# Kernel tuning notes

Measured on AMD Instinct MI355X. Metric: run time of the kernel, lower is better.

Reference implementation:

```python
import jax, jax.numpy as jnp
import numpy as np
from jax import lax

B_, L_, EMB, VOCAB, NL, NH, CH = 4, 2048, 256, 256, 2, 8, 64
D_INNER = 2 * EMB          # expand=2
D_STATE = EMB              # d_state=emb_dim per source
D_CONV = 4
CONV_DIM = D_INNER + 2 * D_STATE
D_PROJ = 2 * D_INNER + 2 * D_STATE + NH
OUT_DIM = 256
EPS = 1e-5


def rms_norm(x, w):
    return x * lax.rsqrt(jnp.mean(x * x, axis=-1, keepdims=True) + EPS) * w


def segsum(a):
    # a: [..., T] -> [..., T, T] with entry (i,j) = sum a[j+1..i], -inf above diag
    T = a.shape[-1]
    cs = jnp.cumsum(a, axis=-1)
    seg = cs[..., :, None] - cs[..., None, :]
    mask = jnp.tril(jnp.ones((T, T), bool))
    return jnp.where(mask, seg, -jnp.inf)


def ssd(x, A, Bm, Cm, chunk):
    # x: [b,l,h,p], A: [b,l,h], Bm/Cm: [b,l,n] (ngroups=1, broadcast over heads)
    b, l, h, p = x.shape
    c = l // chunk
    x = x.reshape(b, c, chunk, h, p)
    A = A.reshape(b, c, chunk, h).transpose(0, 3, 1, 2)  # b h c l
    Bm = Bm.reshape(b, c, chunk, -1)
    Cm = Cm.reshape(b, c, chunk, -1)
    A_cs = jnp.cumsum(A, axis=-1)                        # b h c l
    L = jnp.exp(segsum(A))                               # b h c l l
    Y_diag = jnp.einsum("bcln,bcsn,bhcls,bcshp->bclhp", Cm, Bm, L, x)
    decay_states = jnp.exp(A_cs[..., -1:] - A_cs)        # b h c l
    states = jnp.einsum("bcln,bhcl,bclhp->bchpn", Bm, decay_states, x)
    states = jnp.concatenate([jnp.zeros_like(states[:, :1]), states], axis=1)  # b c+1 h p n
    decay_chunk = jnp.exp(segsum(jnp.pad(A_cs[:, :, :, -1], ((0, 0), (0, 0), (1, 0)))))  # b h c+1 c+1
    new_states = jnp.einsum("bhzc,bchpn->bzhpn", decay_chunk, states)
    states = new_states[:, :-1]                          # b c h p n
    Y_off = jnp.einsum("bcln,bchpn,bhcl->bclhp", Cm, states, jnp.exp(A_cs))
    return (Y_diag + Y_off).reshape(b, l, h, p)


def mamba2_block(u, in_proj_w, conv_w, conv_b, dt_bias, A_log, D, gnorm_w, outp_w):
    b, l, _ = u.shape
    zxbcdt = u @ in_proj_w                               # [b,l,D_PROJ]
    z = zxbcdt[..., :D_INNER]
    xBC = zxbcdt[..., D_INNER:D_INNER + CONV_DIM]
    dt = jax.nn.softplus(zxbcdt[..., -NH:] + dt_bias)    # [b,l,h]
    # causal depthwise conv1d, kernel 4
    xc = lax.conv_general_dilated(
        xBC.transpose(0, 2, 1), conv_w[:, None, :], (1,), [(D_CONV - 1, 0)],
        feature_group_count=CONV_DIM, dimension_numbers=("NCH", "OIH", "NCH"))
    xBC = jax.nn.silu(xc.transpose(0, 2, 1) + conv_b)
    xh = xBC[..., :D_INNER].reshape(b, l, NH, -1)        # [b,l,h,p]
    Bm = xBC[..., D_INNER:D_INNER + D_STATE]
    Cm = xBC[..., D_INNER + D_STATE:]
    A = -jnp.exp(A_log)                                  # [h]
    y = ssd(xh * dt[..., None], A * dt, Bm, Cm, CH)
    y = y + xh * D[:, None]
    y = y.reshape(b, l, D_INNER)
    y = rms_norm(y * jax.nn.silu(z), gnorm_w)
    return y @ outp_w


def _forward(idx, emb, in_proj_w, conv_w, conv_b, dt_bias, A_log, D,
             gnorm_w, outp_w, norm_w, normf_w, head_w):
    h = emb[idx]
    for i in range(NL):
        y = mamba2_block(rms_norm(h, norm_w[i]), in_proj_w[i], conv_w[i], conv_b[i],
                         dt_bias[i], A_log[i], D[i], gnorm_w[i], outp_w[i])
        h = y + h
    h = rms_norm(h, normf_w)
    return h @ head_w


def setup_inputs() -> dict:
    key = jax.random.key(0)
    ks = jax.random.split(key, 13)
    s = 0.02
    return {
        "x": jax.random.uniform(ks[0], (B_, L_, 1), jnp.float32),
        "emb": jax.random.normal(ks[1], (VOCAB, EMB)) * s,
        "in_proj_w": jax.random.normal(ks[2], (NL, EMB, D_PROJ)) * s,
        "conv_w": jax.random.normal(ks[3], (NL, CONV_DIM, D_CONV)) * 0.2,
        "conv_b": jax.random.normal(ks[4], (NL, CONV_DIM)) * s,
        "dt_bias": jax.random.normal(ks[5], (NL, NH)) * 0.1,
        "A_log": jnp.log(jax.random.uniform(ks[6], (NL, NH), minval=0.5, maxval=8.0)),
        "D": jax.random.normal(ks[7], (NL, NH)) * 0.5,
        "gnorm_w": 1.0 + jax.random.normal(ks[8], (NL, D_INNER)) * s,
        "outp_w": jax.random.normal(ks[9], (NL, D_INNER, EMB)) * s,
        "norm_w": 1.0 + jax.random.normal(ks[10], (NL, EMB)) * s,
        "normf_w": 1.0 + jax.random.normal(ks[11], (EMB,)) * s,
        "head_w": jax.random.normal(ks[12], (EMB, OUT_DIM)) * s,
    }


def reference(x, emb, in_proj_w, conv_w, conv_b, dt_bias, A_log, D,
              gnorm_w, outp_w, norm_w, normf_w, head_w):
    idx = jnp.clip(((VOCAB - 1) * x).astype(jnp.int32).squeeze(-1), 0, VOCAB - 1)
    return _forward(idx, emb, in_proj_w, conv_w, conv_b, dt_bias, A_log, D,
                    gnorm_w, outp_w, norm_w, normf_w, head_w)
```

## Files before the change

kernel.cpp:

```cpp
#include <hip/hip_runtime.h>
#include <cstddef>

#define NB 4
#define LSEQ 2048
#define BL (NB*LSEQ)
#define EMBD 256
#define DPROJ 1544
#define ZSTR 1600
#define DIN 512
#define DSTATE 256
#define CONVD 1024
#define NHD 8
#define PD 64
#define NC 32
#define NLAY 2
#define EPS 1e-5f

typedef __bf16 bf16x8 __attribute__((ext_vector_type(8)));
typedef float f32x4 __attribute__((ext_vector_type(4)));
typedef unsigned short u16;

__device__ float g_h [(size_t)BL*EMBD];
__device__ u16   g_ub[(size_t)BL*EMBD];
__device__ float g_zx[(size_t)BL*ZSTR];
__device__ u16   g_xbcb[(size_t)BL*CONVD];
__device__ float g_dt[(size_t)BL*NHD];
__device__ float g_acs[(size_t)NB*NHD*LSEQ];
__device__ float g_dAl[(size_t)NB*NHD*NC];
__device__ float g_y [(size_t)BL*DIN];
__device__ u16   g_yb[(size_t)BL*DIN];
__device__ u16   g_Sb[(size_t)NB*NC*NHD*PD*DSTATE];
__device__ u16   g_wt1[(size_t)ZSTR*EMBD];
__device__ u16   g_wt2[(size_t)EMBD*DIN];
__device__ u16   g_wt3[(size_t)EMBD*EMBD];

__device__ inline u16 f2b(float f){
  unsigned u = __float_as_uint(f);
  return (u16)((u + 0x7fffu + ((u>>16)&1u)) >> 16);
}
__device__ inline float b2f(u16 v){
  return __uint_as_float(((unsigned)v) << 16);
}

__global__ void k_embed(const float* __restrict__ x, const float* __restrict__ emb) {
  int i = blockIdx.x*256 + threadIdx.x;
  int row = i >> 8, col = i & 255;
  int idx = (int)(255.0f * x[row]);
  idx = idx < 0 ? 0 : (idx > 255 ? 255 : idx);
  g_h[i] = emb[idx*EMBD + col];
}

__global__ void k_rmsnorm(const float* __restrict__ in, const float* __restrict__ w,
                          u16* __restrict__ out) {
  int row = blockIdx.x, t = threadIdx.x;
  float v = in[(size_t)row*EMBD + t];
  float ss = v*v;
  #pragma unroll
  for (int o=32;o>0;o>>=1) ss += __shfl_down(ss,o,64);
  __shared__ float ls[4];
  if ((t&63)==0) ls[t>>6]=ss;
  __syncthreads();
  float tot = ls[0]+ls[1]+ls[2]+ls[3];
  float r = rsqrtf(tot*(1.0f/EMBD) + EPS);
  out[(size_t)row*EMBD + t] = f2b(v*r*w[t]);
}

__global__ void k_wt(const float* __restrict__ W, u16* __restrict__ WT, int K, int N) {
  __shared__ float t[64][65];
  int n0 = blockIdx.x*64, k0 = blockIdx.y*64;
  int tid = threadIdx.x;
  #pragma unroll
  for (int e=0;e<16;e++){
    int idx = tid + e*256;
    int kk = idx>>6, nn = idx&63;
    t[kk][nn] = (n0+nn < N) ? W[(size_t)(k0+kk)*N + n0+nn] : 0.f;
  }
  __syncthreads();
  #pragma unroll
  for (int e=0;e<16;e++){
    int idx = tid + e*256;
    int nn = idx>>6, kk = idx&63;
    WT[(size_t)(n0+nn)*K + k0+kk] = f2b(t[kk][nn]);
  }
}

template<int K, bool RES>
__global__ __launch_bounds__(256) void k_mfma_gemm(
    const u16* __restrict__ A, const u16* __restrict__ WT,
    const float* __restrict__ addC, float* __restrict__ C, int nstride)
{
  __shared__ u16 sA[128*64];
  __shared__ u16 sB[64*64];
  const int tid = threadIdx.x;
  const int lane = tid & 63;
  const int w = tid >> 6;
  const int bm = blockIdx.y * 128;
  const int bn = blockIdx.x * 64;
  const int r15 = lane & 15, kg = lane >> 4;
  f32x4 acc[2][4] = {};
  for (int k0 = 0; k0 < K; k0 += 64) {
    #pragma unroll
    for (int it = 0; it < 4; ++it) {
      int ch = it*256 + tid;
      int row = ch >> 3, c16 = ch & 7;
      uint4 v = *(const uint4*)(A + (size_t)(bm+row)*K + k0 + c16*8);
      *(uint4*)(sA + row*64 + ((c16 ^ (row&7))*8)) = v;
    }
    #pragma unroll
    for (int it = 0; it < 2; ++it) {
      int ch = it*256 + tid;
      int row = ch >> 3, c16 = ch & 7;
      uint4 v = *(const uint4*)(WT + (size_t)(bn+row)*K + k0 + c16*8);
      *(uint4*)(sB + row*64 + ((c16 ^ (row&7))*8)) = v;
    }
    __syncthreads();
    #pragma unroll
    for (int ks = 0; ks < 2; ++ks) {
      bf16x8 af[2], bfr[4];
      #pragma unroll
      for (int mr = 0; mr < 2; ++mr) {
        int row = w*32 + mr*16 + r15;
        int c16 = ks*4 + kg;
        af[mr] = *(const bf16x8*)(sA + row*64 + ((c16 ^ (row&7))*8));
      }
      #pragma unroll
      for (int nr = 0; nr < 4; ++nr) {
        int row = nr*16 + r15;
        int c16 = ks*4 + kg;
        bfr[nr] = *(const bf16x8*)(sB + row*64 + ((c16 ^ (row&7))*8));
      }
      #pragma unroll
      for (int mr = 0; mr < 2; ++mr)
        #pragma unroll
        for (int nr = 0; nr < 4; ++nr)
          acc[mr][nr] = __builtin_amdgcn_mfma_f32_16x16x32_bf16(af[mr], bfr[nr], acc[mr][nr], 0, 0, 0);
    }
    __syncthreads();
  }
  #pragma unroll
  for (int mr = 0; mr < 2; ++mr)
    #pragma unroll
    for (int j = 0; j < 4; ++j) {
      int grow = bm + w*32 + mr*16 + (lane>>4)*4 + j;
      #pragma unroll
      for (int nr = 0; nr < 4; ++nr) {
        int gcol = bn + nr*16 + (lane & 15);
        float v = acc[mr][nr][j];
        if (RES) v += addC[(size_t)grow*nstride + gcol];
        C[(size_t)grow*nstride + gcol] = v;
      }
    }
}

__global__ void k_dtscan(const float* __restrict__ dtb, const float* __restrict__ alog) {
  int gid = blockIdx.x;
  int cix = gid & (NC-1), bh = gid >> 5;
  int b = bh >> 3, h = bh & 7;
  int t = threadIdx.x;
  int row = b*LSEQ + cix*64 + t;
  float v = g_zx[(size_t)row*ZSTR + 1536 + h] + dtb[h];
  float sp = (v > 20.f) ? v : log1pf(__expf(v));
  g_dt[(size_t)row*NHD + h] = sp;
  float a = -__expf(alog[h]) * sp;
  #pragma unroll
  for (int o=1;o<64;o<<=1){
    float p = __shfl_up(a,o,64);
    if (t>=o) a += p;
  }
  g_acs[(size_t)bh*LSEQ + cix*64 + t] = a;
  if (t==63) g_dAl[(size_t)bh*NC + cix] = a;
}

__global__ __launch_bounds__(256) void k_conv(const float* __restrict__ cw,
                                              const float* __restrict__ cb) {
  int r0 = blockIdx.x * 4;
  int t0 = r0 & (LSEQ-1);
  int c  = threadIdx.x * 4;
  f32x4 v[7];
  #pragma unroll
  for (int i = 0; i < 7; ++i) {
    int tr = t0 - 3 + i;
    if (tr >= 0)
      v[i] = *(const f32x4*)(&g_zx[(size_t)(r0-3+i)*ZSTR + DIN + c]);
    else
      v[i] = (f32x4){0.f,0.f,0.f,0.f};
  }
  f32x4 w0 = *(const f32x4*)(&cw[(c+0)*4]);
  f32x4 w1 = *(const f32x4*)(&cw[(c+1)*4]);
  f32x4 w2 = *(const f32x4*)(&cw[(c+2)*4]);
  f32x4 w3 = *(const f32x4*)(&cw[(c+3)*4]);
  f32x4 bi = *(const f32x4*)(&cb[c]);
  #pragma unroll
  for (int j = 0; j < 4; ++j) {
    float o[4];
    #pragma unroll
    for (int ch = 0; ch < 4; ++ch) {
      const f32x4& wv = (ch==0)?w0:(ch==1)?w1:(ch==2)?w2:w3;
      float acc = bi[ch];
      #pragma unroll
      for (int k = 0; k < 4; ++k) acc += wv[k] * v[j+k][ch];
      o[ch] = acc / (1.f + __expf(-acc));
    }
    u16 o16[4];
    #pragma unroll
    for (int ch = 0; ch < 4; ++ch) o16[ch] = f2b(o[ch]);
    *(uint2*)(&g_xbcb[(size_t)(r0+j)*CONVD + c]) = *(const uint2*)o16;
  }
}

__global__ __launch_bounds__(512) void k_ssd1(const float* __restrict__ Dp) {
  int g = blockIdx.x;
  int h = g & 7, bc = g >> 3;
  int b = bc >> 5, cix = bc & 31;
  int row0 = b*LSEQ + cix*64;
  int bh = b*NHD + h;
  int tid = threadIdx.x;
  int lane = tid & 63, w = tid >> 6;
  int r15 = lane & 15, kq = lane >> 4;

  __shared__ u16 sBmt[256*64];
  __shared__ u16 sXt [64*64];
  __shared__ u16 sXdt[64*64];
  __shared__ u16 sM  [64*64];
  __shared__ float sAc[64];

  {
    int l = tid & 63;
    #pragma unroll
    for (int it = 0; it < 4; ++it) {
      int nc = (tid >> 6) + it*8;
      uint4 v4 = *(const uint4*)(&g_xbcb[(size_t)(row0+l)*CONVD + 512 + nc*8]);
      const u16* hp = (const u16*)&v4;
      #pragma unroll
      for (int i = 0; i < 8; ++i) {
        int n = nc*8 + i;
        sBmt[n*64 + (((l>>3) ^ (n&7))<<3) + (l&7)] = hp[i];
      }
    }
  }
  {
    int s = tid & 63, pc = tid >> 6;
    float ac  = g_acs[(size_t)bh*LSEQ + cix*64 + s];
    float dal = g_dAl[(size_t)bh*NC + cix];
    float dtv = g_dt[(size_t)(row0+s)*NHD + h];
    float dec = __expf(dal - ac);
    if (pc == 0) sAc[s] = ac;
    uint4 v4 = *(const uint4*)(&g_xbcb[(size_t)(row0+s)*CONVD + h*64 + pc*8]);
    const u16* hp = (const u16*)&v4;
    #pragma unroll
    for (int i = 0; i < 8; ++i) {
      int p = pc*8 + i;
      float xv = b2f(hp[i]) * dtv;
      int sw = (((s>>3) ^ (p&7))<<3) + (s&7);
      sXt [p*64 + sw] = f2b(xv);
      sXdt[p*64 + sw] = f2b(xv*dec);
    }
  }
  __syncthreads();

  {
    int S0  = (w >> 1)*16;
    int L0a = ((2*w) & 3)*16, L0b = L0a + 16;
    f32x4 acc0 = {}, acc1 = {};
    const u16* Ab = &g_xbcb[(size_t)(row0+S0 +r15)*CONVD + 512];
    const u16* B0 = &g_xbcb[(size_t)(row0+L0a+r15)*CONVD + 768];
    const u16* B1 = &g_xbcb[(size_t)(row0+L0b+r15)*CONVD + 768];
    #pragma unroll
    for (int ks = 0; ks < 8; ++ks) {
      int off = (ks*4 + kq)*8;
      bf16x8 af = *(const bf16x8*)(Ab + off);
      bf16x8 b0 = *(const bf16x8*)(B0 + off);
      bf16x8 b1 = *(const bf16x8*)(B1 + off);
      acc0 = __builtin_amdgcn_mfma_f32_16x16x32_bf16(af, b0, acc0, 0, 0, 0);
      acc1 = __builtin_amdgcn_mfma_f32_16x16x32_bf16(af, b1, acc1, 0, 0, 0);
    }
    int l0 = L0a + r15, l1 = L0b + r15;
    float acl0 = sAc[l0], acl1 = sAc[l1];
    #pragma unroll
    for (int j = 0; j < 4; ++j) {
      int s_ = S0 + kq*4 + j;
      float acs_ = sAc[s_];
      float m0 = (s_ <= l0) ? acc0[j]*__expf(acl0 - acs_) : 0.f;
      float m1 = (s_ <= l1) ? acc1[j]*__expf(acl1 - acs_) : 0.f;
      sM[l0*64 + (((s_>>3) ^ (l0&7))<<3) + (s_&7)] = f2b(m0);
      sM[l1*64 + (((s_>>3) ^ (l1&7))<<3) + (s_&7)] = f2b(m1);
    }
  }
  __syncthreads();

  {
    int lt = w >> 1;
    int pt0 = (2*w) & 3;
    int L0 = lt*16, P0 = pt0*16;
    f32x4 acc0 = {}, acc1 = {};
    #pragma unroll
    for (int ks = 0; ks < 2; ++ks) {
      int ch = ks*4 + kq;
      int sw = (ch ^ (r15&7))<<3;
      bf16x8 af = *(const bf16x8*)(&sM [(L0+r15)*64 + sw]);
      bf16x8 b0 = *(const bf16x8*)(&sXt[(P0+r15)*64 + sw]);
      bf16x8 b1 = *(const bf16x8*)(&sXt[(P0+16+r15)*64 + sw]);
      acc0 = __builtin_amdgcn_mfma_f32_16x16x32_bf16(af, b0, acc0, 0, 0, 0);
      acc1 = __builtin_amdgcn_mfma_f32_16x16x32_bf16(af, b1, acc1, 0, 0, 0);
    }
    float Dv = Dp[h];
    #pragma unroll
    for (int j = 0; j < 4; ++j) {
      int l = L0 + kq*4 + j;
      int p0 = P0 + r15, p1 = p0 + 16;
      float xh0 = b2f(g_xbcb[(size_t)(row0+l)*CONVD + h*64 + p0]);
      float xh1 = b2f(g_xbcb[(size_t)(row0+l)*CONVD + h*64 + p1]);
      g_y[(size_t)(row0+l)*DIN + h*64 + p0] = acc0[j] + Dv*xh0;
      g_y[(size_t)(row0+l)*DIN + h*64 + p1] = acc1[j] + Dv*xh1;
    }
  }

  {
    int P0 = (w >> 1)*16;
    int N0 = (w & 1)*128;
    f32x4 acc[8] = {};
    #pragma unroll
    for (int ks = 0; ks < 2; ++ks) {
      int ch = ks*4 + kq;
      int sw = (ch ^ (r15&7))<<3;
      bf16x8 af = *(const bf16x8*)(&sXdt[(P0+r15)*64 + sw]);
      #pragma unroll
      for (int nt = 0; nt < 8; ++nt) {
        bf16x8 bf = *(const bf16x8*)(&sBmt[(N0+nt*16+r15)*64 + sw]);
        acc[nt] = __builtin_amdgcn_mfma_f32_16x16x32_bf16(af, bf, acc[nt], 0, 0, 0);
      }
    }
    size_t Sbase = ((size_t)(bc*NHD + h))*PD*DSTATE;
    #pragma unroll
    for (int nt = 0; nt < 8; ++nt)
      #pragma unroll
      for (int j = 0; j < 4; ++j) {
        int p = P0 + kq*4 + j;
        int n = N0 + nt*16 + r15;
        g_Sb[Sbase + (size_t)p*DSTATE + n] = f2b(acc[nt][j]);
      }
  }
}

__global__ void k_sscan() {
  int i = blockIdx.x*256 + threadIdx.x;
  int pn = i & (PD*DSTATE-1);
  int bh = i >> 14;
  int b = bh >> 3, h = bh & 7;
  float carry = 0.f;
  for (int c=0;c<NC;c++){
    size_t off = ((size_t)((b*NC+c)*NHD + h))*PD*DSTATE + pn;
    float cur = b2f(g_Sb[off]);
    g_Sb[off] = f2b(carry);
    carry = carry*__expf(g_dAl[(size_t)(b*NHD+h)*NC + c]) + cur;
  }
}

__global__ __launch_bounds__(256) void k_ssd2() {
  int g = blockIdx.x;
  int h = g & 7, bc = g >> 3;
  int b = bc >> 5, cix = bc & 31;
  int row0 = b*LSEQ + cix*64;
  int bh = b*NHD + h;
  int tid = threadIdx.x;
  int lane = tid & 63, w = tid >> 6;
  int r15 = lane & 15, kq = lane >> 4;
  __shared__ u16 sSb[64*256];
  __shared__ float sAc[64];
  size_t Sbase = ((size_t)(bc*NHD + h))*PD*DSTATE;
  #pragma unroll
  for (int it = 0; it < 8; ++it) {
    int e = tid + it*256;
    int c16 = e & 31, p = e >> 5;
    uint4 v4 = *(const uint4*)(&g_Sb[Sbase + (size_t)p*DSTATE + c16*8]);
    *(uint4*)(&sSb[p*256 + ((c16 ^ (p&7))<<3)]) = v4;
  }
  if (tid < 64) sAc[tid] = g_acs[(size_t)bh*LSEQ + cix*64 + tid];
  __syncthreads();
  int L0 = w*16;
  const u16* Ab = &g_xbcb[(size_t)(row0+L0+r15)*CONVD + 768];
  f32x4 acc[4] = {};
  #pragma unroll
  for (int ks = 0; ks < 8; ++ks) {
    int ch = ks*4 + kq;
    bf16x8 af = *(const bf16x8*)(Ab + ch*8);
    #pragma unroll
    for (int pt = 0; pt < 4; ++pt) {
      bf16x8 bf = *(const bf16x8*)(&sSb[(pt*16+r15)*256 + ((ch ^ (r15&7))<<3)]);
      acc[pt] = __builtin_amdgcn_mfma_f32_16x16x32_bf16(af, bf, acc[pt], 0, 0, 0);
    }
  }
  #pragma unroll
  for (int j = 0; j < 4; ++j) {
    int l = L0 + kq*4 + j;
    float ev = __expf(sAc[l]);
    #pragma unroll
    for (int pt = 0; pt < 4; ++pt) {
      int p = pt*16 + r15;
      g_y[(size_t)(row0+l)*DIN + h*64 + p] += ev*acc[pt][j];
    }
  }
}

__global__ void k_gated(const float* __restrict__ gw) {
  int row = blockIdx.x, t = threadIdx.x;
  float v[2]; float ss = 0.f;
  #pragma unroll
  for (int e=0;e<2;e++){
    int c = t + e*256;
    float z = g_zx[(size_t)row*ZSTR + c];
    float val = g_y[(size_t)row*DIN + c] * (z/(1.f+__expf(-z)));
    v[e]=val; ss += val*val;
  }
  #pragma unroll
  for (int o=32;o>0;o>>=1) ss += __shfl_down(ss,o,64);
  __shared__ float ls[4];
  if ((t&63)==0) ls[t>>6]=ss;
  __syncthreads();
  float tot = ls[0]+ls[1]+ls[2]+ls[3];
  float r = rsqrtf(tot*(1.f/DIN) + EPS);
  #pragma unroll
  for (int e=0;e<2;e++){
    int c = t+e*256;
    g_yb[(size_t)row*DIN + c] = f2b(v[e]*r*gw[c]);
  }
}

extern "C" void kernel_launch(void* const* d_in, const int* in_sizes, int n_in,
                              void* d_out, int out_size, void* d_ws, size_t ws_size,
                              hipStream_t stream) {
  const float* x     = (const float*)d_in[0];
  const float* emb   = (const float*)d_in[1];
  const float* inpw  = (const float*)d_in[2];
  const float* convw = (const float*)d_in[3];
  const float* convb = (const float*)d_in[4];
  const float* dtb   = (const float*)d_in[5];
  const float* alog  = (const float*)d_in[6];
  const float* Dp    = (const float*)d_in[7];
  const float* gnw   = (const float*)d_in[8];
  const float* outw  = (const float*)d_in[9];
  const float* normw = (const float*)d_in[10];
  const float* normf = (const float*)d_in[11];
  const float* headw = (const float*)d_in[12];
  float* out = (float*)d_out;
  (void)in_sizes; (void)n_in; (void)out_size; (void)d_ws; (void)ws_size;

  float *ph, *pzx;
  u16 *pub, *pyb, *pwt1, *pwt2, *pwt3;
  hipGetSymbolAddress((void**)&ph,   HIP_SYMBOL(g_h));
  hipGetSymbolAddress((void**)&pub,  HIP_SYMBOL(g_ub));
  hipGetSymbolAddress((void**)&pzx,  HIP_SYMBOL(g_zx));
  hipGetSymbolAddress((void**)&pyb,  HIP_SYMBOL(g_yb));
  hipGetSymbolAddress((void**)&pwt1, HIP_SYMBOL(g_wt1));
  hipGetSymbolAddress((void**)&pwt2, HIP_SYMBOL(g_wt2));
  hipGetSymbolAddress((void**)&pwt3, HIP_SYMBOL(g_wt3));

  k_embed<<<BL*EMBD/256, 256, 0, stream>>>(x, emb);
  for (int i=0;i<NLAY;i++){
    k_rmsnorm<<<BL, 256, 0, stream>>>(ph, normw + i*EMBD, pub);
    k_wt<<<dim3(ZSTR/64, EMBD/64), 256, 0, stream>>>(inpw + (size_t)i*EMBD*DPROJ, pwt1, EMBD, DPROJ);
    k_mfma_gemm<EMBD,false><<<dim3(ZSTR/64, BL/128), 256, 0, stream>>>(pub, pwt1, nullptr, pzx, ZSTR);
    k_dtscan<<<NB*NHD*NC, 64, 0, stream>>>(dtb + i*NHD, alog + i*NHD);
    k_conv<<<BL/4, 256, 0, stream>>>(convw + i*CONVD*4, convb + i*CONVD);
    k_ssd1<<<NB*NC*NHD, 512, 0, stream>>>(Dp + i*NHD);
    k_sscan<<<(NB*NHD*PD*DSTATE)/256, 256, 0, stream>>>();
    k_ssd2<<<NB*NC*NHD, 256, 0, stream>>>();
    k_gated<<<BL, 256, 0, stream>>>(gnw + i*DIN);
    k_wt<<<dim3(EMBD/64, DIN/64), 256, 0, stream>>>(outw + (size_t)i*DIN*EMBD, pwt2, DIN, EMBD);
    k_mfma_gemm<DIN,true><<<dim3(EMBD/64, BL/128), 256, 0, stream>>>(pyb, pwt2, ph, ph, EMBD);
  }
  k_rmsnorm<<<BL, 256, 0, stream>>>(ph, normf, pub);
  k_wt<<<dim3(EMBD/64, EMBD/64), 256, 0, stream>>>(headw, pwt3, EMBD, EMBD);
  k_mfma_gemm<EMBD,false><<<dim3(EMBD/64, BL/128), 256, 0, stream>>>(pub, pwt3, nullptr, out, EMBD);
}
```

Baseline: 388.2 us.

## Emit transposed SSD operands from conv kernel and read MFMA operands from global

The conv kernel now also writes pre-transposed, dt-scaled and decay-scaled copies of x and a transposed B matrix into new global buffers. The first SSD kernel then reads its MFMA operands straight from global memory instead of transposing them into shared memory, and the second SSD kernel likewise reads the state matrix from global memory without staging it in LDS. This removes the LDS staging, scattered 16-bit transpose stores and one barrier phase, and cuts shared memory use. In exchange the conv kernel does extra global writes with small 8-byte strided stores, and the MFMA operand loads now hit global or L2 memory rather than LDS.

```diff
diff --git a/kernel.cpp b/kernel.cpp
--- a/kernel.cpp
+++ b/kernel.cpp
@@ -30,6 +30,9 @@
 __device__ float g_y [(size_t)BL*DIN];
 __device__ u16   g_yb[(size_t)BL*DIN];
 __device__ u16   g_Sb[(size_t)NB*NC*NHD*PD*DSTATE];
+__device__ u16   g_bmt[(size_t)NB*NC*DSTATE*64];
+__device__ u16   g_xht[(size_t)NB*NC*NHD*PD*64];
+__device__ u16   g_xdt[(size_t)NB*NC*NHD*PD*64];
 __device__ u16   g_wt1[(size_t)ZSTR*EMBD];
 __device__ u16   g_wt2[(size_t)EMBD*DIN];
 __device__ u16   g_wt3[(size_t)EMBD*EMBD];
@@ -190,21 +193,58 @@
   f32x4 w2 = *(const f32x4*)(&cw[(c+2)*4]);
   f32x4 w3 = *(const f32x4*)(&cw[(c+3)*4]);
   f32x4 bi = *(const f32x4*)(&cb[c]);
+  float ov[4][4];
+  u16 o16[4][4];
   #pragma unroll
   for (int j = 0; j < 4; ++j) {
-    float o[4];
     #pragma unroll
     for (int ch = 0; ch < 4; ++ch) {
       const f32x4& wv = (ch==0)?w0:(ch==1)?w1:(ch==2)?w2:w3;
       float acc = bi[ch];
       #pragma unroll
       for (int k = 0; k < 4; ++k) acc += wv[k] * v[j+k][ch];
-      o[ch] = acc / (1.f + __expf(-acc));
-    }
-    u16 o16[4];
-    #pragma unroll
-    for (int ch = 0; ch < 4; ++ch) o16[ch] = f2b(o[ch]);
-    *(uint2*)(&g_xbcb[(size_t)(r0+j)*CONVD + c]) = *(const uint2*)o16;
+      float s = acc / (1.f + __expf(-acc));
+      ov[j][ch] = s;
+      o16[j][ch] = f2b(s);
+    }
+    *(uint2*)(&g_xbcb[(size_t)(r0+j)*CONVD + c]) = *(const uint2*)(&o16[j][0]);
+  }
+  int b = r0 >> 11, cix = t0 >> 6, l0 = t0 & 63;
+  int bc = b*NC + cix;
+  if (c < DIN) {
+    int h = c >> 6;
+    int bh = b*NHD + h;
+    float dal = g_dAl[(size_t)bh*NC + cix];
+    float dtv[4], dec[4];
+    #pragma unroll
+    for (int j = 0; j < 4; ++j) {
+      float ac = g_acs[(size_t)bh*LSEQ + t0 + j];
+      dtv[j] = g_dt[(size_t)(r0+j)*NHD + h];
+      dec[j] = __expf(dal - ac);
+    }
+    #pragma unroll
+    for (int ch = 0; ch < 4; ++ch) {
+      int p = (c & 63) + ch;
+      u16 xa[4], xd[4];
+      #pragma unroll
+      for (int j = 0; j < 4; ++j) {
+        float xv = ov[j][ch] * dtv[j];
+        xa[j] = f2b(xv);
+        xd[j] = f2b(xv * dec[j]);
+      }
+      size_t base = ((size_t)(bc*NHD + h)*64 + p)*64 + l0;
+      *(uint2*)(&g_xht[base]) = *(const uint2*)xa;
+      *(uint2*)(&g_xdt[base]) = *(const uint2*)xd;
+    }
+  } else if (c < DIN + DSTATE) {
+    #pragma unroll
+    for (int ch = 0; ch < 4; ++ch) {
+      int n = c - DIN + ch;
+      u16 xa[4];
+      #pragma unroll
+      for (int j = 0; j < 4; ++j) xa[j] = o16[j][ch];
+      *(uint2*)(&g_bmt[((size_t)bc*DSTATE + n)*64 + l0]) = *(const uint2*)xa;
+    }
   }
 }
 
@@ -218,44 +258,9 @@
   int lane = tid & 63, w = tid >> 6;
   int r15 = lane & 15, kq = lane >> 4;
 
-  __shared__ u16 sBmt[256*64];
-  __shared__ u16 sXt [64*64];
-  __shared__ u16 sXdt[64*64];
-  __shared__ u16 sM  [64*64];
+  __shared__ u16 sM[64*64];
   __shared__ float sAc[64];
-
-  {
-    int l = tid & 63;
-    #pragma unroll
-    for (int it = 0; it < 4; ++it) {
-      int nc = (tid >> 6) + it*8;
-      uint4 v4 = *(const uint4*)(&g_xbcb[(size_t)(row0+l)*CONVD + 512 + nc*8]);
-      const u16* hp = (const u16*)&v4;
-      #pragma unroll
-      for (int i = 0; i < 8; ++i) {
-        int n = nc*8 + i;
-        sBmt[n*64 + (((l>>3) ^ (n&7))<<3) + (l&7)] = hp[i];
-      }
-    }
-  }
-  {
-    int s = tid & 63, pc = tid >> 6;
-    float ac  = g_acs[(size_t)bh*LSEQ + cix*64 + s];
-    float dal = g_dAl[(size_t)bh*NC + cix];
-    float dtv = g_dt[(size_t)(row0+s)*NHD + h];
-    float dec = __expf(dal - ac);
-    if (pc == 0) sAc[s] = ac;
-    uint4 v4 = *(const uint4*)(&g_xbcb[(size_t)(row0+s)*CONVD + h*64 + pc*8]);
-    const u16* hp = (const u16*)&v4;
-    #pragma unroll
-    for (int i = 0; i < 8; ++i) {
-      int p = pc*8 + i;
-      float xv = b2f(hp[i]) * dtv;
-      int sw = (((s>>3) ^ (p&7))<<3) + (s&7);
-      sXt [p*64 + sw] = f2b(xv);
-      sXdt[p*64 + sw] = f2b(xv*dec);
-    }
-  }
+  if (tid < 64) sAc[tid] = g_acs[(size_t)bh*LSEQ + cix*64 + tid];
   __syncthreads();
 
   {
@@ -289,17 +294,17 @@
   __syncthreads();
 
   {
-    int lt = w >> 1;
-    int pt0 = (2*w) & 3;
-    int L0 = lt*16, P0 = pt0*16;
+    int L0 = (w >> 1)*16;
+    int P0 = ((2*w) & 3)*16;
+    const u16* Xb = &g_xht[(size_t)(bc*NHD + h)*64*64];
     f32x4 acc0 = {}, acc1 = {};
     #pragma unroll
     for (int ks = 0; ks < 2; ++ks) {
       int ch = ks*4 + kq;
       int sw = (ch ^ (r15&7))<<3;
-      bf16x8 af = *(const bf16x8*)(&sM [(L0+r15)*64 + sw]);
-      bf16x8 b0 = *(const bf16x8*)(&sXt[(P0+r15)*64 + sw]);
-      bf16x8 b1 = *(const bf16x8*)(&sXt[(P0+16+r15)*64 + sw]);
+      bf16x8 af = *(const bf16x8*)(&sM[(L0+r15)*64 + sw]);
+      bf16x8 b0 = *(const bf16x8*)(Xb + (size_t)(P0+r15)*64 + ch*8);
+      bf16x8 b1 = *(const bf16x8*)(Xb + (size_t)(P0+16+r15)*64 + ch*8);
       acc0 = __builtin_amdgcn_mfma_f32_16x16x32_bf16(af, b0, acc0, 0, 0, 0);
       acc1 = __builtin_amdgcn_mfma_f32_16x16x32_bf16(af, b1, acc1, 0, 0, 0);
     }
@@ -318,15 +323,16 @@
   {
     int P0 = (w >> 1)*16;
     int N0 = (w & 1)*128;
+    const u16* Ax = &g_xdt[(size_t)(bc*NHD + h)*64*64];
+    const u16* Bb = &g_bmt[(size_t)bc*DSTATE*64];
     f32x4 acc[8] = {};
     #pragma unroll
     for (int ks = 0; ks < 2; ++ks) {
       int ch = ks*4 + kq;
-      int sw = (ch ^ (r15&7))<<3;
-      bf16x8 af = *(const bf16x8*)(&sXdt[(P0+r15)*64 + sw]);
+      bf16x8 af = *(const bf16x8*)(Ax + (size_t)(P0+r15)*64 + ch*8);
       #pragma unroll
       for (int nt = 0; nt < 8; ++nt) {
-        bf16x8 bf = *(const bf16x8*)(&sBmt[(N0+nt*16+r15)*64 + sw]);
+        bf16x8 bf = *(const bf16x8*)(Bb + (size_t)(N0+nt*16+r15)*64 + ch*8);
         acc[nt] = __builtin_amdgcn_mfma_f32_16x16x32_bf16(af, bf, acc[nt], 0, 0, 0);
       }
     }
@@ -365,20 +371,12 @@
   int tid = threadIdx.x;
   int lane = tid & 63, w = tid >> 6;
   int r15 = lane & 15, kq = lane >> 4;
-  __shared__ u16 sSb[64*256];
   __shared__ float sAc[64];
-  size_t Sbase = ((size_t)(bc*NHD + h))*PD*DSTATE;
-  #pragma unroll
-  for (int it = 0; it < 8; ++it) {
-    int e = tid + it*256;
-    int c16 = e & 31, p = e >> 5;
-    uint4 v4 = *(const uint4*)(&g_Sb[Sbase + (size_t)p*DSTATE + c16*8]);
-    *(uint4*)(&sSb[p*256 + ((c16 ^ (p&7))<<3)]) = v4;
-  }
   if (tid < 64) sAc[tid] = g_acs[(size_t)bh*LSEQ + cix*64 + tid];
   __syncthreads();
   int L0 = w*16;
   const u16* Ab = &g_xbcb[(size_t)(row0+L0+r15)*CONVD + 768];
+  const u16* Sb = &g_Sb[((size_t)(bc*NHD + h))*PD*DSTATE];
   f32x4 acc[4] = {};
   #pragma unroll
   for (int ks = 0; ks < 8; ++ks) {
@@ -386,7 +384,7 @@
     bf16x8 af = *(const bf16x8*)(Ab + ch*8);
     #pragma unroll
     for (int pt = 0; pt < 4; ++pt) {
-      bf16x8 bf = *(const bf16x8*)(&sSb[(pt*16+r15)*256 + ((ch ^ (r15&7))<<3)]);
+      bf16x8 bf = *(const bf16x8*)(Sb + (size_t)(pt*16+r15)*DSTATE + ch*8);
       acc[pt] = __builtin_amdgcn_mfma_f32_16x16x32_bf16(af, bf, acc[pt], 0, 0, 0);
     }
   }
```

Measured after the change: 487.8 us. 25.7% more time.
